# Optimization experiments

Hardware: AMD Instinct MI355X
Metric: run time of the kernel (lower is better)

The kernel has to match this reference:

```python
import jax, jax.numpy as jnp
from jax import lax
import numpy as np

# gate config (matches init_kwargs)
TOP_K = 8
N_GROUP = 8
TOPK_GROUP = 4
ROUTED_SCALING_FACTOR = 2.5
NORM_TOPK_PROB = True


def setup_inputs() -> dict:
    key = jax.random.key(0)
    k1, k2, k3 = jax.random.split(key, 3)
    B, S, H, E = 4, 4096, 4096, 256
    x = jax.random.normal(k1, (B, S, H), dtype=jnp.float32)
    weight = jax.random.normal(k2, (E, H), dtype=jnp.float32) * 0.02
    bias = jax.random.normal(k3, (E,), dtype=jnp.float32) * 0.01
    return {"x": x, "weight": weight, "bias": bias}


def reference(x, weight, bias):
    # gate logits: [B, S, E]
    gates = jnp.einsum('bsh,eh->bse', x, weight)
    scores = jax.nn.sigmoid(gates.astype(jnp.float32))
    orig_scores = scores
    s = scores + bias  # biased scores used only for selection

    B, S, E = s.shape
    if N_GROUP > 1:
        Eg = E // N_GROUP
        sg = s.reshape(B, S, N_GROUP, Eg)
        # group score = sum of top-2 expert scores within each group: [B, S, G]
        group_scores = lax.top_k(sg, 2)[0].sum(axis=-1)
        k_drop = N_GROUP - TOPK_GROUP
        # indices of the k_drop lowest-scoring groups
        drop_idx = lax.top_k(-group_scores, k_drop)[1]  # [B, S, k_drop]
        # keep mask over groups: [B, S, G]
        keep = ~jnp.any(drop_idx[..., :, None] == jnp.arange(N_GROUP), axis=-2)
        sg = jnp.where(keep[..., None], sg, 0.0)  # scatter_ 0.0 on dropped groups
        s = sg.reshape(B, S, E)

    # final top-k over masked, biased scores
    inds = lax.top_k(s, TOP_K)[1]  # [B, S, TOP_K]
    sel = jnp.take_along_axis(orig_scores, inds, axis=-1)  # unbiased scores
    if TOP_K > 1 and NORM_TOPK_PROB:
        sel = sel / (sel.sum(axis=-1, keepdims=True) + 1e-20)
    sel = sel * ROUTED_SCALING_FACTOR
    return (inds, sel)
```

## Files before the change

kernel.cpp:

```cpp
#include <hip/hip_runtime.h>
#include <hip/hip_bf16.h>
#include <math.h>

#define HDIM 4096
#define NEXP 256
#define BM   32
#define BK   32
#define TOPK 8
#define NGRP 8
#define DROPG 4

#define XS_PAD 36
#define WS_PAD 260

__global__ __launch_bounds__(256, 2)
void gate_gemm_sigmoid(const float* __restrict__ x,
                       const float* __restrict__ w,
                       float* __restrict__ scores)
{
    __shared__ float xs[BK][XS_PAD];
    __shared__ float wsh[BK][WS_PAD];

    const int tid = threadIdx.x;
    const int tm = tid >> 5;
    const int tn = tid & 31;
    const long m0 = (long)blockIdx.x * BM;

    float acc[4][8];
#pragma unroll
    for (int i = 0; i < 4; ++i)
#pragma unroll
        for (int j = 0; j < 8; ++j) acc[i][j] = 0.f;

    const int xt = tid >> 3;
    const int xk = (tid & 7) * 4;

    for (int k0 = 0; k0 < HDIM; k0 += BK) {
        float4 xv = *reinterpret_cast<const float4*>(
            &x[(m0 + xt) * HDIM + k0 + xk]);
        float4 wv[8];
#pragma unroll
        for (int i = 0; i < 8; ++i) {
            int e = i * 32 + (tid >> 3);
            wv[i] = *reinterpret_cast<const float4*>(
                &w[(long)e * HDIM + k0 + xk]);
        }
        __syncthreads();
        xs[xk + 0][xt] = xv.x;
        xs[xk + 1][xt] = xv.y;
        xs[xk + 2][xt] = xv.z;
        xs[xk + 3][xt] = xv.w;
#pragma unroll
        for (int i = 0; i < 8; ++i) {
            int e = i * 32 + (tid >> 3);
            wsh[xk + 0][e] = wv[i].x;
            wsh[xk + 1][e] = wv[i].y;
            wsh[xk + 2][e] = wv[i].z;
            wsh[xk + 3][e] = wv[i].w;
        }
        __syncthreads();
#pragma unroll
        for (int kk = 0; kk < BK; ++kk) {
            float4 xf = *reinterpret_cast<const float4*>(&xs[kk][tm * 4]);
            float4 w0 = *reinterpret_cast<const float4*>(&wsh[kk][tn * 8]);
            float4 w1 = *reinterpret_cast<const float4*>(&wsh[kk][tn * 8 + 4]);
            float xr[4] = {xf.x, xf.y, xf.z, xf.w};
            float wr[8] = {w0.x, w0.y, w0.z, w0.w, w1.x, w1.y, w1.z, w1.w};
#pragma unroll
            for (int i = 0; i < 4; ++i)
#pragma unroll
                for (int j = 0; j < 8; ++j)
                    acc[i][j] = fmaf(xr[i], wr[j], acc[i][j]);
        }
    }

#pragma unroll
    for (int i = 0; i < 4; ++i) {
        long t = m0 + tm * 4 + i;
        float4 o0, o1;
        o0.x = 1.f / (1.f + expf(-acc[i][0]));
        o0.y = 1.f / (1.f + expf(-acc[i][1]));
        o0.z = 1.f / (1.f + expf(-acc[i][2]));
        o0.w = 1.f / (1.f + expf(-acc[i][3]));
        o1.x = 1.f / (1.f + expf(-acc[i][4]));
        o1.y = 1.f / (1.f + expf(-acc[i][5]));
        o1.z = 1.f / (1.f + expf(-acc[i][6]));
        o1.w = 1.f / (1.f + expf(-acc[i][7]));
        float* dst = &scores[t * NEXP + tn * 8];
        *reinterpret_cast<float4*>(dst)     = o0;
        *reinterpret_cast<float4*>(dst + 4) = o1;
    }
}

__global__ __launch_bounds__(64, 8)
void gate_topk(const float* __restrict__ scores,
               const float* __restrict__ bias,
               float* __restrict__ out_idx,
               float* __restrict__ out_val)
{
    __shared__ float so[NEXP];
    __shared__ float sb[NEXP];
    __shared__ float gsc[NGRP];

    const long t = blockIdx.x;
    const int l = threadIdx.x;

    float bv[4];
    int ce[4];
#pragma unroll
    for (int j = 0; j < 4; ++j) {
        int e = l + 64 * j;
        float s = scores[t * NEXP + e];
        float b = s + bias[e];
        so[e] = s;
        sb[e] = b;
        bv[j] = b;
        ce[j] = e;
    }
    __syncthreads();

    if (l < NGRP) {
        float m1 = -1e30f, m2 = -1e30f;
        int base = l * 32;
        for (int i = 0; i < 32; ++i) {
            float v = sb[base + i];
            if (v > m1) { m2 = m1; m1 = v; }
            else if (v > m2) { m2 = v; }
        }
        gsc[l] = m1 + m2;
    }
    __syncthreads();

    float g[8];
#pragma unroll
    for (int i = 0; i < 8; ++i) g[i] = gsc[i];
    unsigned dropped = 0;
    for (int it = 0; it < DROPG; ++it) {
        float mn = 1e38f; int mi = 0;
#pragma unroll
        for (int i = 0; i < 8; ++i) {
            bool alive = !((dropped >> i) & 1);
            if (alive && g[i] < mn) { mn = g[i]; mi = i; }
        }
        dropped |= 1u << mi;
    }

    float cv[4];
#pragma unroll
    for (int j = 0; j < 4; ++j) {
        int grp = ce[j] >> 5;
        cv[j] = ((dropped >> grp) & 1) ? 0.0f : bv[j];
    }

    int ind[8];
#pragma unroll
    for (int r = 0; r < TOPK; ++r) {
        float lv = -1e38f; int li = 0x7fffffff;
#pragma unroll
        for (int j = 0; j < 4; ++j) {
            if (cv[j] > lv || (cv[j] == lv && ce[j] < li)) { lv = cv[j]; li = ce[j]; }
        }
#pragma unroll
        for (int off = 32; off >= 1; off >>= 1) {
            float ov = __shfl_xor(lv, off);
            int   oi = __shfl_xor(li, off);
            if (ov > lv || (ov == lv && oi < li)) { lv = ov; li = oi; }
        }
        ind[r] = li;
#pragma unroll
        for (int j = 0; j < 4; ++j)
            if (ce[j] == li) cv[j] = -1e38f;
    }

    int myi = 0;
#pragma unroll
    for (int r = 0; r < TOPK; ++r)
        if (l == r) myi = ind[r];
    float sv = (l < TOPK) ? so[myi] : 0.f;
    float sum = sv;
#pragma unroll
    for (int off = 1; off < TOPK; off <<= 1)
        sum += __shfl_xor(sum, off);
    if (l < TOPK) {
        out_idx[t * TOPK + l] = (float)myi;
        out_val[t * TOPK + l] = sv / (sum + 1e-20f) * 2.5f;
    }
}

extern "C" void kernel_launch(void* const* d_in, const int* in_sizes, int n_in,
                              void* d_out, int out_size, void* d_ws, size_t ws_size,
                              hipStream_t stream) {
    const float* x    = (const float*)d_in[0];
    const float* w    = (const float*)d_in[1];
    const float* bias = (const float*)d_in[2];

    const int ntok = in_sizes[0] / HDIM;

    float* scores = (float*)d_ws;
    float* out_i  = (float*)d_out;
    float* out_v  = (float*)d_out + (long)ntok * TOPK;

    gate_gemm_sigmoid<<<ntok / BM, 256, 0, stream>>>(x, w, scores);
    gate_topk<<<ntok, 64, 0, stream>>>(scores, bias, out_i, out_v);
}
```

Before: 837.7 us.

## Use split-bf16 MFMA gate GEMM with split-K and fp32 refinement of ambiguous tokens

Replaces the scalar FP32 GEMM with a bf16x3 (hi/lo split) MFMA GEMM. Weights are pre-converted into a tiled bf16 layout and loaded directly to LDS, and the K dimension is split in two with partial sums written to a workspace. The top-k kernel now processes four tokens per block, sums the partials, applies the sigmoid and uses wave shuffles for group scores. Tokens whose top-k or group-selection margins fall below a threshold are flagged and recomputed in exact FP32 by a refine kernel. This aims to move the dominant GEMM onto matrix cores while keeping selection exact, at the cost of extra kernels, partial-sum traffic and a hardcoded token count.

```diff
diff --git a/kernel.cpp b/kernel.cpp
--- a/kernel.cpp
+++ b/kernel.cpp
@@ -1,189 +1,313 @@
 #include <hip/hip_runtime.h>
 #include <hip/hip_bf16.h>
 #include <math.h>
-
-#define HDIM 4096
-#define NEXP 256
-#define BM   32
-#define BK   32
-#define TOPK 8
-#define NGRP 8
-#define DROPG 4
-
-#define XS_PAD 36
-#define WS_PAD 260
+#include <stdint.h>
+
+#define HDIM   4096
+#define NEXP   256
+#define TOPK   8
+#define NGRP   8
+#define NTOK   16384
+#define KSPLIT 2
+#define BM     64
+#define BK     32
+#define KCHUNKS (HDIM/BK)
+#define NIT    ((HDIM/KSPLIT)/BK)
+#define TAU    2.5e-5f
+#define TAUG   5.0e-5f
+
+typedef __attribute__((ext_vector_type(8))) short short8v;
+typedef __attribute__((ext_vector_type(4))) float f32x4;
+
+#define WS_WSPLIT  (2ull*NTOK*NEXP*4)
+#define WS_CTR     (WS_WSPLIT + 4ull*1024*1024)
+#define WS_LIST    (WS_CTR + 256)
+
+__device__ inline void gload_lds16(const void* g, void* l) {
+    __builtin_amdgcn_global_load_lds(
+        (const __attribute__((address_space(1))) unsigned int*)g,
+        (__attribute__((address_space(3))) unsigned int*)l, 16, 0, 0);
+}
+
+__device__ inline unsigned rtn16(unsigned u) {
+    return (u + 0x7fffu + ((u >> 16) & 1u)) >> 16;
+}
+
+__global__ __launch_bounds__(256)
+void convert_w(const float* __restrict__ w, unsigned short* __restrict__ wws)
+{
+    int gid  = blockIdx.x * 256 + threadIdx.x;
+    int e    = gid >> 9;
+    int cell = gid & 511;
+    int kc = cell >> 2, kb = cell & 3;
+    const float* src = w + (size_t)e * HDIM + cell * 8;
+    float4 f0 = *(const float4*)src;
+    float4 f1 = *(const float4*)(src + 4);
+    float fs[8] = {f0.x,f0.y,f0.z,f0.w,f1.x,f1.y,f1.z,f1.w};
+    unsigned hw[4], lw[4];
+#pragma unroll
+    for (int p = 0; p < 4; ++p) {
+        unsigned u0 = __float_as_uint(fs[2*p]);
+        unsigned u1 = __float_as_uint(fs[2*p+1]);
+        unsigned h0 = rtn16(u0), h1 = rtn16(u1);
+        float r0 = fs[2*p]   - __uint_as_float(h0 << 16);
+        float r1 = fs[2*p+1] - __uint_as_float(h1 << 16);
+        unsigned l0 = rtn16(__float_as_uint(r0));
+        unsigned l1 = rtn16(__float_as_uint(r1));
+        hw[p] = h0 | (h1 << 16);
+        lw[p] = l0 | (l1 << 16);
+    }
+    size_t bh = ((size_t)(kc*2 + 0)*4 + kb)*2048 + e*8;
+    size_t blo= ((size_t)(kc*2 + 1)*4 + kb)*2048 + e*8;
+    *(uint4*)&wws[bh]  = make_uint4(hw[0],hw[1],hw[2],hw[3]);
+    *(uint4*)&wws[blo] = make_uint4(lw[0],lw[1],lw[2],lw[3]);
+}
 
 __global__ __launch_bounds__(256, 2)
-void gate_gemm_sigmoid(const float* __restrict__ x,
-                       const float* __restrict__ w,
-                       float* __restrict__ scores)
-{
-    __shared__ float xs[BK][XS_PAD];
-    __shared__ float wsh[BK][WS_PAD];
-
-    const int tid = threadIdx.x;
-    const int tm = tid >> 5;
-    const int tn = tid & 31;
-    const long m0 = (long)blockIdx.x * BM;
-
-    float acc[4][8];
-#pragma unroll
-    for (int i = 0; i < 4; ++i)
-#pragma unroll
-        for (int j = 0; j < 8; ++j) acc[i][j] = 0.f;
-
-    const int xt = tid >> 3;
-    const int xk = (tid & 7) * 4;
-
-    for (int k0 = 0; k0 < HDIM; k0 += BK) {
-        float4 xv = *reinterpret_cast<const float4*>(
-            &x[(m0 + xt) * HDIM + k0 + xk]);
-        float4 wv[8];
-#pragma unroll
-        for (int i = 0; i < 8; ++i) {
-            int e = i * 32 + (tid >> 3);
-            wv[i] = *reinterpret_cast<const float4*>(
-                &w[(long)e * HDIM + k0 + xk]);
-        }
+void gate_gemm(const float* __restrict__ x, const unsigned short* __restrict__ wws,
+               float* __restrict__ partials)
+{
+    __shared__ uint4 ldsv[2560];
+    char* lds = (char*)ldsv;
+    const int t = threadIdx.x;
+    const int wid = t >> 6, lane = t & 63;
+    const int mb = blockIdx.x & 255, ks = blockIdx.x >> 8;
+    const size_t m0 = (size_t)mb * BM;
+    const int frow = lane & 15, fkb = lane >> 4;
+    const int srow = t & 63, skb = t >> 6;
+
+    f32x4 acc[4][4];
+#pragma unroll
+    for (int m = 0; m < 4; ++m)
+#pragma unroll
+        for (int n = 0; n < 4; ++n) acc[m][n] = (f32x4){0.f,0.f,0.f,0.f};
+
+    const float* xrow = x + (m0 + srow) * HDIM + ks * (HDIM/KSPLIT) + skb * 8;
+    const char* wbase = (const char*)wws + (size_t)(ks * (KCHUNKS/KSPLIT)) * 32768;
+
+    float4 xa = *(const float4*)(xrow);
+    float4 xb = *(const float4*)(xrow + 4);
+
+    for (int it = 0; it < NIT; ++it) {
         __syncthreads();
-        xs[xk + 0][xt] = xv.x;
-        xs[xk + 1][xt] = xv.y;
-        xs[xk + 2][xt] = xv.z;
-        xs[xk + 3][xt] = xv.w;
-#pragma unroll
-        for (int i = 0; i < 8; ++i) {
-            int e = i * 32 + (tid >> 3);
-            wsh[xk + 0][e] = wv[i].x;
-            wsh[xk + 1][e] = wv[i].y;
-            wsh[xk + 2][e] = wv[i].z;
-            wsh[xk + 3][e] = wv[i].w;
+        {
+            float fs[8] = {xa.x,xa.y,xa.z,xa.w,xb.x,xb.y,xb.z,xb.w};
+            unsigned hw[4], lw[4];
+#pragma unroll
+            for (int p = 0; p < 4; ++p) {
+                unsigned u0 = __float_as_uint(fs[2*p]);
+                unsigned u1 = __float_as_uint(fs[2*p+1]);
+                hw[p] = (u0 >> 16) | (u1 & 0xffff0000u);
+                float r0 = fs[2*p]   - __uint_as_float(u0 & 0xffff0000u);
+                float r1 = fs[2*p+1] - __uint_as_float(u1 & 0xffff0000u);
+                unsigned l0 = rtn16(__float_as_uint(r0));
+                unsigned l1 = rtn16(__float_as_uint(r1));
+                lw[p] = l0 | (l1 << 16);
+            }
+            *(uint4*)&lds[skb*1024 + srow*16]        = make_uint4(hw[0],hw[1],hw[2],hw[3]);
+            *(uint4*)&lds[4096 + skb*1024 + srow*16] = make_uint4(lw[0],lw[1],lw[2],lw[3]);
+        }
+        {
+            const char* wsrc = wbase + (size_t)it * 32768;
+#pragma unroll
+            for (int j = 0; j < 8; ++j) {
+                int chunk = wid * 8 + j;
+                gload_lds16(wsrc + chunk*1024 + lane*16, &lds[8192 + chunk*1024]);
+            }
         }
         __syncthreads();
-#pragma unroll
-        for (int kk = 0; kk < BK; ++kk) {
-            float4 xf = *reinterpret_cast<const float4*>(&xs[kk][tm * 4]);
-            float4 w0 = *reinterpret_cast<const float4*>(&wsh[kk][tn * 8]);
-            float4 w1 = *reinterpret_cast<const float4*>(&wsh[kk][tn * 8 + 4]);
-            float xr[4] = {xf.x, xf.y, xf.z, xf.w};
-            float wr[8] = {w0.x, w0.y, w0.z, w0.w, w1.x, w1.y, w1.z, w1.w};
-#pragma unroll
-            for (int i = 0; i < 4; ++i)
-#pragma unroll
-                for (int j = 0; j < 8; ++j)
-                    acc[i][j] = fmaf(xr[i], wr[j], acc[i][j]);
-        }
-    }
-
-#pragma unroll
-    for (int i = 0; i < 4; ++i) {
-        long t = m0 + tm * 4 + i;
-        float4 o0, o1;
-        o0.x = 1.f / (1.f + expf(-acc[i][0]));
-        o0.y = 1.f / (1.f + expf(-acc[i][1]));
-        o0.z = 1.f / (1.f + expf(-acc[i][2]));
-        o0.w = 1.f / (1.f + expf(-acc[i][3]));
-        o1.x = 1.f / (1.f + expf(-acc[i][4]));
-        o1.y = 1.f / (1.f + expf(-acc[i][5]));
-        o1.z = 1.f / (1.f + expf(-acc[i][6]));
-        o1.w = 1.f / (1.f + expf(-acc[i][7]));
-        float* dst = &scores[t * NEXP + tn * 8];
-        *reinterpret_cast<float4*>(dst)     = o0;
-        *reinterpret_cast<float4*>(dst + 4) = o1;
-    }
-}
-
-__global__ __launch_bounds__(64, 8)
-void gate_topk(const float* __restrict__ scores,
-               const float* __restrict__ bias,
-               float* __restrict__ out_idx,
-               float* __restrict__ out_val)
-{
-    __shared__ float so[NEXP];
-    __shared__ float sb[NEXP];
-    __shared__ float gsc[NGRP];
-
-    const long t = blockIdx.x;
-    const int l = threadIdx.x;
-
-    float bv[4];
-    int ce[4];
+        if (it + 1 < NIT) {
+            xa = *(const float4*)(xrow + (it+1)*BK);
+            xb = *(const float4*)(xrow + (it+1)*BK + 4);
+        }
+        short8v ah[4], al[4];
+#pragma unroll
+        for (int m = 0; m < 4; ++m) {
+            ah[m] = *(const short8v*)&lds[        fkb*1024 + (m*16+frow)*16];
+            al[m] = *(const short8v*)&lds[4096 +  fkb*1024 + (m*16+frow)*16];
+        }
+#pragma unroll
+        for (int n = 0; n < 4; ++n) {
+            int col = wid*64 + n*16 + frow;
+            short8v bh = *(const short8v*)&lds[8192 +         fkb*4096 + col*16];
+            short8v bl = *(const short8v*)&lds[8192 + 16384 + fkb*4096 + col*16];
+#pragma unroll
+            for (int m = 0; m < 4; ++m)
+                acc[m][n] = __builtin_amdgcn_mfma_f32_16x16x32_bf16(ah[m], bh, acc[m][n], 0,0,0);
+#pragma unroll
+            for (int m = 0; m < 4; ++m)
+                acc[m][n] = __builtin_amdgcn_mfma_f32_16x16x32_bf16(ah[m], bl, acc[m][n], 0,0,0);
+#pragma unroll
+            for (int m = 0; m < 4; ++m)
+                acc[m][n] = __builtin_amdgcn_mfma_f32_16x16x32_bf16(al[m], bh, acc[m][n], 0,0,0);
+        }
+    }
+    float* pb = partials + (size_t)ks * NTOK * NEXP;
+#pragma unroll
+    for (int m = 0; m < 4; ++m)
+#pragma unroll
+        for (int n = 0; n < 4; ++n) {
+            int col = wid*64 + n*16 + (lane & 15);
+#pragma unroll
+            for (int r = 0; r < 4; ++r) {
+                size_t row = m0 + m*16 + (lane >> 4)*4 + r;
+                pb[row*NEXP + col] = acc[m][n][r];
+            }
+        }
+}
+
+__device__ void wave_gate_topk(float* gb , float* ss ,
+                               const float* __restrict__ bias, int lane, size_t tok,
+                               float* __restrict__ oIdx, float* __restrict__ oVal,
+                               unsigned* flagCtr, int* flagList)
+{
+    float bv[4]; int ce[4];
 #pragma unroll
     for (int j = 0; j < 4; ++j) {
-        int e = l + 64 * j;
-        float s = scores[t * NEXP + e];
+        int e = lane + 64*j;
+        float s = 1.f / (1.f + expf(-gb[e]));
         float b = s + bias[e];
-        so[e] = s;
-        sb[e] = b;
-        bv[j] = b;
-        ce[j] = e;
-    }
-    __syncthreads();
-
-    if (l < NGRP) {
-        float m1 = -1e30f, m2 = -1e30f;
-        int base = l * 32;
-        for (int i = 0; i < 32; ++i) {
-            float v = sb[base + i];
-            if (v > m1) { m2 = m1; m1 = v; }
-            else if (v > m2) { m2 = v; }
-        }
-        gsc[l] = m1 + m2;
-    }
-    __syncthreads();
-
-    float g[8];
-#pragma unroll
-    for (int i = 0; i < 8; ++i) g[i] = gsc[i];
-    unsigned dropped = 0;
-    for (int it = 0; it < DROPG; ++it) {
+        ss[e] = s; gb[e] = b;
+        bv[j] = b; ce[j] = e;
+    }
+    int g = lane >> 3;
+    float4 gv = *(const float4*)(gb + g*32 + (lane & 7)*4);
+    float a1 = fmaxf(gv.x,gv.y), a2 = fminf(gv.x,gv.y);
+    float b1 = fmaxf(gv.z,gv.w), b2 = fminf(gv.z,gv.w);
+    float m1 = fmaxf(a1,b1);
+    float m2 = fmaxf(fminf(a1,b1), fmaxf(a2,b2));
+#pragma unroll
+    for (int off = 1; off < 8; off <<= 1) {
+        float om1 = __shfl_xor(m1, off), om2 = __shfl_xor(m2, off);
+        float n1 = fmaxf(m1, om1);
+        float n2 = fmaxf(fminf(m1, om1), fmaxf(m2, om2));
+        m1 = n1; m2 = n2;
+    }
+    float gs = m1 + m2;
+    float gsc[8];
+#pragma unroll
+    for (int i = 0; i < 8; ++i) gsc[i] = __shfl(gs, i*8);
+    unsigned dropped = 0; float lastdrop = 0.f;
+#pragma unroll
+    for (int itd = 0; itd < 4; ++itd) {
         float mn = 1e38f; int mi = 0;
 #pragma unroll
-        for (int i = 0; i < 8; ++i) {
-            bool alive = !((dropped >> i) & 1);
-            if (alive && g[i] < mn) { mn = g[i]; mi = i; }
-        }
-        dropped |= 1u << mi;
-    }
+        for (int i = 0; i < 8; ++i)
+            if (!((dropped >> i) & 1) && gsc[i] < mn) { mn = gsc[i]; mi = i; }
+        dropped |= 1u << mi; lastdrop = mn;
+    }
+    float minkeep = 1e38f;
+#pragma unroll
+    for (int i = 0; i < 8; ++i)
+        if (!((dropped >> i) & 1)) minkeep = fminf(minkeep, gsc[i]);
+    float gmargin = minkeep - lastdrop;
 
     float cv[4];
 #pragma unroll
-    for (int j = 0; j < 4; ++j) {
-        int grp = ce[j] >> 5;
-        cv[j] = ((dropped >> grp) & 1) ? 0.0f : bv[j];
-    }
-
-    int ind[8];
-#pragma unroll
-    for (int r = 0; r < TOPK; ++r) {
+    for (int j = 0; j < 4; ++j)
+        cv[j] = ((dropped >> (ce[j] >> 5)) & 1) ? 0.0f : bv[j];
+
+    float vals[9]; int ind[9];
+#pragma unroll
+    for (int r = 0; r < 9; ++r) {
         float lv = -1e38f; int li = 0x7fffffff;
 #pragma unroll
-        for (int j = 0; j < 4; ++j) {
+        for (int j = 0; j < 4; ++j)
             if (cv[j] > lv || (cv[j] == lv && ce[j] < li)) { lv = cv[j]; li = ce[j]; }
-        }
 #pragma unroll
         for (int off = 32; off >= 1; off >>= 1) {
             float ov = __shfl_xor(lv, off);
             int   oi = __shfl_xor(li, off);
             if (ov > lv || (ov == lv && oi < li)) { lv = ov; li = oi; }
         }
-        ind[r] = li;
+        vals[r] = lv; ind[r] = li;
 #pragma unroll
         for (int j = 0; j < 4; ++j)
             if (ce[j] == li) cv[j] = -1e38f;
     }
+    float mingap = 1e38f;
+#pragma unroll
+    for (int r = 0; r < 8; ++r) mingap = fminf(mingap, vals[r] - vals[r+1]);
 
     int myi = 0;
 #pragma unroll
-    for (int r = 0; r < TOPK; ++r)
-        if (l == r) myi = ind[r];
-    float sv = (l < TOPK) ? so[myi] : 0.f;
+    for (int r = 0; r < 8; ++r) if (lane == r) myi = ind[r];
+    float sv = (lane < 8) ? ss[myi] : 0.f;
     float sum = sv;
 #pragma unroll
-    for (int off = 1; off < TOPK; off <<= 1)
-        sum += __shfl_xor(sum, off);
-    if (l < TOPK) {
-        out_idx[t * TOPK + l] = (float)myi;
-        out_val[t * TOPK + l] = sv / (sum + 1e-20f) * 2.5f;
+    for (int off = 1; off < 8; off <<= 1) sum += __shfl_xor(sum, off);
+    if (lane < 8) {
+        oIdx[tok*8 + lane] = (float)myi;
+        oVal[tok*8 + lane] = sv / (sum + 1e-20f) * 2.5f;
+    }
+    if (flagCtr && lane == 0 && (mingap < TAU || gmargin < TAUG)) {
+        unsigned p = atomicAdd(flagCtr, 1u);
+        flagList[p] = (int)tok;
+    }
+}
+
+__global__ __launch_bounds__(256, 4)
+void gate_topk(const float* __restrict__ partials, const float* __restrict__ bias,
+               float* __restrict__ oIdx, float* __restrict__ oVal,
+               unsigned* ctr, int* list)
+{
+    __shared__ float gb[4][256];
+    __shared__ float ss[4][256];
+    int wid = threadIdx.x >> 6, lane = threadIdx.x & 63;
+    size_t tok = (size_t)blockIdx.x * 4 + wid;
+    const float* p0 = partials + tok * NEXP;
+    const float* p1 = partials + (size_t)NTOK * NEXP + tok * NEXP;
+#pragma unroll
+    for (int j = 0; j < 4; ++j) {
+        int e = lane + 64*j;
+        gb[wid][e] = p0[e] + p1[e];
+    }
+    wave_gate_topk(gb[wid], ss[wid], bias, lane, tok, oIdx, oVal, ctr, list);
+}
+
+__global__ __launch_bounds__(256, 2)
+void gate_refine(const float* __restrict__ x, const float* __restrict__ w,
+                 const float* __restrict__ bias,
+                 float* __restrict__ oIdx, float* __restrict__ oVal,
+                 const unsigned* __restrict__ ctr, const int* __restrict__ list)
+{
+    __shared__ float gb[4][256];
+    __shared__ float ss[4][256];
+    int nf = (int)*ctr;
+    int nb = (nf + 3) >> 2;
+    int e = threadIdx.x;
+    int wid = threadIdx.x >> 6, lane = threadIdx.x & 63;
+    for (int batch = blockIdx.x; batch < nb; batch += gridDim.x) {
+        int tcount = nf - batch*4; if (tcount > 4) tcount = 4;
+        int tk[4];
+#pragma unroll
+        for (int i = 0; i < 4; ++i) {
+            int ii = i < tcount ? i : tcount - 1;
+            tk[i] = list[batch*4 + ii];
+        }
+        const float* wr = w + (size_t)e * HDIM;
+        const float* x0 = x + (size_t)tk[0] * HDIM;
+        const float* x1 = x + (size_t)tk[1] * HDIM;
+        const float* x2 = x + (size_t)tk[2] * HDIM;
+        const float* x3 = x + (size_t)tk[3] * HDIM;
+        float a0=0.f, a1=0.f, a2=0.f, a3=0.f;
+        for (int k = 0; k < HDIM; k += 4) {
+            float4 wv = *(const float4*)(wr + k);
+            float4 v0 = *(const float4*)(x0 + k);
+            float4 v1 = *(const float4*)(x1 + k);
+            float4 v2 = *(const float4*)(x2 + k);
+            float4 v3 = *(const float4*)(x3 + k);
+            a0 += wv.x*v0.x + wv.y*v0.y + wv.z*v0.z + wv.w*v0.w;
+            a1 += wv.x*v1.x + wv.y*v1.y + wv.z*v1.z + wv.w*v1.w;
+            a2 += wv.x*v2.x + wv.y*v2.y + wv.z*v2.z + wv.w*v2.w;
+            a3 += wv.x*v3.x + wv.y*v3.y + wv.z*v3.z + wv.w*v3.w;
+        }
+        __syncthreads();
+        gb[0][e] = a0; gb[1][e] = a1; gb[2][e] = a2; gb[3][e] = a3;
+        __syncthreads();
+        if (wid < tcount)
+            wave_gate_topk(gb[wid], ss[wid], bias, lane, (size_t)tk[wid],
+                           oIdx, oVal, nullptr, nullptr);
     }
 }
 
@@ -193,13 +317,19 @@
     const float* x    = (const float*)d_in[0];
     const float* w    = (const float*)d_in[1];
     const float* bias = (const float*)d_in[2];
-
     const int ntok = in_sizes[0] / HDIM;
 
-    float* scores = (float*)d_ws;
-    float* out_i  = (float*)d_out;
-    float* out_v  = (float*)d_out + (long)ntok * TOPK;
-
-    gate_gemm_sigmoid<<<ntok / BM, 256, 0, stream>>>(x, w, scores);
-    gate_topk<<<ntok, 64, 0, stream>>>(scores, bias, out_i, out_v);
-}
+    char* ws = (char*)d_ws;
+    float* partials      = (float*)ws;
+    unsigned short* wws  = (unsigned short*)(ws + WS_WSPLIT);
+    unsigned* ctr        = (unsigned*)(ws + WS_CTR);
+    int* list            = (int*)(ws + WS_LIST);
+    float* oIdx = (float*)d_out;
+    float* oVal = (float*)d_out + (size_t)ntok * TOPK;
+
+    hipMemsetAsync(ctr, 0, 4, stream);
+    convert_w <<<512, 256, 0, stream>>>(w, wws);
+    gate_gemm <<<(ntok/BM) * KSPLIT, 256, 0, stream>>>(x, wws, partials);
+    gate_topk <<<ntok/4, 256, 0, stream>>>(partials, bias, oIdx, oVal, ctr, list);
+    gate_refine<<<256, 256, 0, stream>>>(x, w, bias, oIdx, oVal, ctr, list);
+}
```

New measurement: 782.3 us. -6.6%, faster.
